# Optimization experiments

Measured on AMD Instinct MI355X. Metric: run time of the kernel, lower is better.

The kernel has to match this reference:

```python
import jax, jax.numpy as jnp
from jax import lax
import numpy as np

NEG = -1e30  # log-space -inf surrogate (avoids inf-inf NaNs)

def setup_inputs() -> dict:
    key = jax.random.key(0)
    k1, k2, k3, k4 = jax.random.split(key, 4)
    B, T, V, L = 32, 1024, 1024, 128
    logits = jax.random.normal(k1, (B, T, V), dtype=jnp.float32)
    targets = jax.random.randint(k2, (B, L), 1, V, dtype=jnp.int32)  # blank=0 excluded
    targets_lengths = jax.random.randint(k3, (B,), 64, L + 1, dtype=jnp.int32)
    logits_lengths = jax.random.randint(k4, (B,), 512, T + 1, dtype=jnp.int32)
    return {"logits": logits, "targets": targets,
            "logits_lengths": logits_lengths, "targets_lengths": targets_lengths}

def _ctc_neg_log_likelihood(logits, targets, logits_lengths, targets_lengths):
    # warp-ctc semantics: softmax applied internally, blank label = 0,
    # returns per-example negative log likelihood (reduce=False).
    B, T, V = logits.shape
    L = targets.shape[1]
    S = 2 * L + 1  # extended label seq: blank, l1, blank, l2, ..., blank
    logp = jax.nn.log_softmax(logits, axis=-1)            # [B,T,V]
    ext = jnp.zeros((B, S), jnp.int32).at[:, 1::2].set(targets)  # blanks at even s
    lp = jnp.take_along_axis(logp, ext[:, None, :], axis=2)      # [B,T,S]

    s_idx = jnp.arange(S)
    valid_s = s_idx[None, :] < (2 * targets_lengths[:, None] + 1)  # ragged label mask
    # skip transition s-2 -> s allowed only at non-blank s with ext[s] != ext[s-2]
    ext_m2 = jnp.pad(ext, ((0, 0), (2, 0)), constant_values=-1)[:, :S]
    can_skip = (s_idx[None, :] % 2 == 1) & (ext != ext_m2)

    alpha0 = jnp.full((B, S), NEG, logits.dtype)
    alpha0 = alpha0.at[:, 0].set(lp[:, 0, 0]).at[:, 1].set(lp[:, 0, 1])
    alpha0 = jnp.where(valid_s, alpha0, NEG)

    def step(alpha, inp):
        lp_t, t = inp  # lp_t: [B,S]
        a1 = alpha
        a2 = jnp.pad(alpha[:, :-1], ((0, 0), (1, 0)), constant_values=NEG)
        a3 = jnp.where(can_skip,
                       jnp.pad(alpha[:, :-2], ((0, 0), (2, 0)), constant_values=NEG),
                       NEG)
        m = jnp.maximum(jnp.maximum(a1, a2), a3)
        new = m + jnp.log(jnp.exp(a1 - m) + jnp.exp(a2 - m) + jnp.exp(a3 - m)) + lp_t
        new = jnp.where(valid_s, new, NEG)
        # freeze alpha past each example's logit length (ragged time)
        new = jnp.where((t < logits_lengths)[:, None], new, alpha)
        return new, None

    lp_time = jnp.swapaxes(lp, 0, 1)  # [T,B,S]
    alpha_T, _ = lax.scan(step, alpha0, (lp_time[1:], jnp.arange(1, T)))
    end_blank = jnp.take_along_axis(alpha_T, (2 * targets_lengths)[:, None], axis=1)[:, 0]
    end_label = jnp.take_along_axis(alpha_T, (2 * targets_lengths - 1)[:, None], axis=1)[:, 0]
    return -jnp.logaddexp(end_blank, end_label)  # [B]

def reference(logits, targets, logits_lengths, targets_lengths):
    return _ctc_neg_log_likelihood(logits, targets, logits_lengths, targets_lengths)
```

## Files before the change

kernel.cpp:

```cpp
#include <hip/hip_runtime.h>


#define LOG2E 1.4426950408889634f
#define LN2   0.6931471805599453f

constexpr int B = 32, T = 1024, V = 1024, L = 128;
constexpr int S = 2 * L + 1;
constexpr int TS = 64;

__device__ inline float fexp2(float x) { return __builtin_amdgcn_exp2f(x); }
__device__ inline float flog2(float x) { return __builtin_amdgcn_logf(x); }

template<int CTRL>
__device__ inline float dpp_mov(float old_, float x) {
    return __int_as_float(__builtin_amdgcn_update_dpp(
        __float_as_int(old_), __float_as_int(x), CTRL, 0xF, 0xF, false));
}

__global__ __launch_bounds__(256) void k_lse_gather(
    const float* __restrict__ logits, const int* __restrict__ targets,
    const int* __restrict__ tgtlen,
    float* __restrict__ pQ, float* __restrict__ pB)
{
    const int row = blockIdx.x;
    const int b   = row >> 10;
    const float* x = logits + (size_t)row * V;
    const int tid = threadIdx.x;

    float4 v = reinterpret_cast<const float4*>(x)[tid];
    float m = fmaxf(fmaxf(v.x, v.y), fmaxf(v.z, v.w));
    #pragma unroll
    for (int off = 32; off; off >>= 1) m = fmaxf(m, __shfl_xor(m, off));

    __shared__ float red[8];
    const int lane = tid & 63, wv = tid >> 6;
    if (lane == 0) red[wv] = m;
    __syncthreads();
    m = fmaxf(fmaxf(red[0], red[1]), fmaxf(red[2], red[3]));

    float s = fexp2((v.x - m) * LOG2E) + fexp2((v.y - m) * LOG2E)
            + fexp2((v.z - m) * LOG2E) + fexp2((v.w - m) * LOG2E);
    #pragma unroll
    for (int off = 32; off; off >>= 1) s += __shfl_xor(s, off);
    if (lane == 0) red[4 + wv] = s;
    __syncthreads();
    s = red[4] + red[5] + red[6] + red[7];

    const float lse2 = m * LOG2E + flog2(s);
    if (tid == 0) {
        pB[row] = fexp2(x[0] * LOG2E - lse2);
    } else if (tid <= L) {
        const int j  = tid - 1;
        const int tl = tgtlen[b];
        const int lab = targets[b * L + j];
        pQ[(size_t)row * 128 + j] =
            (j < tl) ? fexp2(x[lab] * LOG2E - lse2) : 0.0f;
    }
}

__global__ __launch_bounds__(64) void k_ctc_alpha(
    const float* __restrict__ pQ, const float* __restrict__ pB,
    const int* __restrict__ targets, const int* __restrict__ loglen,
    const int* __restrict__ tgtlen, float* __restrict__ out)
{
    const int b  = blockIdx.x;
    const int l  = threadIdx.x;
    const int len = loglen[b];
    const int tl  = tgtlen[b];

    const int* tg = targets + b * L;
    const int t2l   = tg[2 * l];
    const int t2lm1 = (l > 0) ? tg[2 * l - 1] : -3;
    const int t2lp1 = tg[2 * l + 1];
    const bool cs1 = (t2l != t2lm1);
    const bool cs3 = (t2lp1 != t2l);

    float A0 = (l == 0) ? pB[(size_t)b * T] : 0.0f;
    float A1 = (l == 0) ? pQ[(size_t)b * T * 128] : 0.0f;
    float A2 = 0.0f, A3 = 0.0f, A4 = 0.0f;
    float p3 = 0.0f;
    int Se = 0;

    __shared__ __align__(16) float sQ[2][TS][128];
    __shared__ __align__(16) float sB[2][TS];
    __shared__ float alpha[S];

    const float* gQ = pQ + (size_t)b * T * 128 + (l & 31) * 4;

    #define STAGE(buf, t0)                                                     \
    {                                                                          \
        _Pragma("unroll")                                                      \
        for (int c = 0; c < TS / 2; ++c) {                                     \
            const int r  = (t0) + 2 * c + (l >> 5);                            \
            const int rc = (r < T) ? r : (T - 1);                              \
            const float* gp = gQ + (size_t)rc * 128;                           \
            __builtin_amdgcn_global_load_lds(                                  \
                (const __attribute__((address_space(1))) void*)gp,             \
                (__attribute__((address_space(3))) void*)&sQ[buf][2 * c][0],   \
                16, 0, 0);                                                     \
        }                                                                      \
        {                                                                      \
            const int r  = (t0) + l;                                           \
            const int rc = (r < T) ? r : (T - 1);                              \
            const float* gp = pB + (size_t)b * T + rc;                         \
            __builtin_amdgcn_global_load_lds(                                  \
                (const __attribute__((address_space(1))) void*)gp,             \
                (__attribute__((address_space(3))) void*)&sB[buf][0],          \
                4, 0, 0);                                                      \
        }                                                                      \
    }

    float2 qa[8]; float ba[8];
    float2 qb[8]; float bbf[8];

    #define LOADG(QD, BD, cbuf, r0)                                            \
    {                                                                          \
        _Pragma("unroll")                                                      \
        for (int r = 0; r < 8; ++r) {                                          \
            QD[r] = *reinterpret_cast<const float2*>(&sQ[cbuf][(r0) + r][2*l]);\
            BD[r] = sB[cbuf][(r0) + r];                                        \
        }                                                                      \
    }

    #define STEP_ONE(pb, p1, pl3)                                              \
    {                                                                          \
        const float n0 = (A0 + p3) * (pb);                                     \
        const float n1 = (A1 + A0 + (cs1 ? p3 : 0.0f)) * (p1);                 \
        const float n2 = (A2 + A1) * (pb);                                     \
        const float n3 = (A3 + A2 + (cs3 ? A1 : 0.0f)) * (pl3);                \
        const float n4 = (A4 + A3) * (pb);                                     \
        A0 = n0; A1 = n1; A2 = n2; A3 = n3; A4 = n4;                           \
        p3 = dpp_mov<0x138>(0.0f, A3);             \
    }

    #define RESCALE()                                                          \
    {                                                                          \
        float m_ = fmaxf(fmaxf(A0, A1), fmaxf(A2, fmaxf(A3, A4)));             \
        m_ = fmaxf(m_, dpp_mov<0x111>(m_, m_));                \
        m_ = fmaxf(m_, dpp_mov<0x112>(m_, m_));                \
        m_ = fmaxf(m_, dpp_mov<0x114>(m_, m_));                \
        m_ = fmaxf(m_, dpp_mov<0x118>(m_, m_));                \
        m_ = fmaxf(m_, dpp_mov<0x142>(m_, m_));              \
        m_ = fmaxf(m_, dpp_mov<0x143>(m_, m_));              \
        const int e = (__builtin_amdgcn_readlane(__float_as_int(m_), 63)       \
                       >> 23) & 0xff;                                          \
        int kb = 374 - e;                       \
        if (kb > 254) kb = 254;                      \
        const float sc = __int_as_float(kb << 23);                             \
        A0 *= sc; A1 *= sc; A2 *= sc; A3 *= sc; A4 *= sc; p3 *= sc;            \
        Se -= (kb - 127);                                                      \
    }

    STAGE(0, 1);
    int cb = 0;

    int tb = 1;
    for (; tb + TS <= len; tb += TS) {
        asm volatile("s_waitcnt vmcnt(0)" ::: "memory");
        STAGE(cb ^ 1, tb + TS);
        LOADG(qa, ba, cb, 0);
        #pragma unroll
        for (int g = 0; g < 8; ++g) {
            if (g < 7) {
                if (g & 1) { LOADG(qa, ba, cb, (g + 1) * 8); }
                else       { LOADG(qb, bbf, cb, (g + 1) * 8); }
            }
            #pragma unroll
            for (int i = 0; i < 8; ++i) {
                if (g & 1) { STEP_ONE(bbf[i], qb[i].x, qb[i].y); }
                else       { STEP_ONE(ba[i],  qa[i].x, qa[i].y); }
            }
            RESCALE();
        }
        cb ^= 1;
    }
    if (tb < len) {
        asm volatile("s_waitcnt vmcnt(0)" ::: "memory");
        LOADG(qa, ba, cb, 0);
        #pragma unroll
        for (int g = 0; g < 8; ++g) {
            if (g < 7) {
                if (g & 1) { LOADG(qa, ba, cb, (g + 1) * 8); }
                else       { LOADG(qb, bbf, cb, (g + 1) * 8); }
            }
            #pragma unroll
            for (int i = 0; i < 8; ++i) {
                if (tb + g * 8 + i < len) {
                    if (g & 1) { STEP_ONE(bbf[i], qb[i].x, qb[i].y); }
                    else       { STEP_ONE(ba[i],  qa[i].x, qa[i].y); }
                }
            }
            if (tb + g * 8 + 7 < len) RESCALE();
        }
    }
    #undef STEP_ONE
    #undef RESCALE
    #undef LOADG
    #undef STAGE

    alpha[4 * l + 0] = A0;
    alpha[4 * l + 1] = A1;
    alpha[4 * l + 2] = A2;
    alpha[4 * l + 3] = A3;
    if (l == 63) alpha[256] = A4;
    __syncthreads();

    if (l == 0) {
        const float sum = alpha[2 * tl] + alpha[2 * tl - 1];
        out[b] = -LN2 * (flog2(sum) + (float)Se);
    }
}

extern "C" void kernel_launch(void* const* d_in, const int* in_sizes, int n_in,
                              void* d_out, int out_size, void* d_ws, size_t ws_size,
                              hipStream_t stream) {
    const float* logits  = (const float*)d_in[0];
    const int*   targets = (const int*)d_in[1];
    const int*   loglen  = (const int*)d_in[2];
    const int*   tgtlen  = (const int*)d_in[3];
    float* out = (float*)d_out;
    float* pQ = (float*)d_ws;
    float* pB = pQ + (size_t)B * T * 128;

    k_lse_gather<<<B * T, 256, 0, stream>>>(logits, targets, tgtlen, pQ, pB);
    k_ctc_alpha<<<B, 64, 0, stream>>>(pQ, pB, targets, loglen, tgtlen, out);
}
```

Before: 94.07 us.

## Pack eight batch recurrences per block and shrink the staging tile

```diff
diff --git a/kernel.cpp b/kernel.cpp
--- a/kernel.cpp
+++ b/kernel.cpp
@@ -6,7 +6,8 @@
 
 constexpr int B = 32, T = 1024, V = 1024, L = 128;
 constexpr int S = 2 * L + 1;
-constexpr int TS = 64;
+constexpr int TS = 16;
+constexpr int WPB = 8;
 
 __device__ inline float fexp2(float x) { return __builtin_amdgcn_exp2f(x); }
 __device__ inline float flog2(float x) { return __builtin_amdgcn_logf(x); }
@@ -58,13 +59,18 @@
     }
 }
 
-__global__ __launch_bounds__(64) void k_ctc_alpha(
+__global__ __launch_bounds__(512) void k_ctc_alpha(
     const float* __restrict__ pQ, const float* __restrict__ pB,
     const int* __restrict__ targets, const int* __restrict__ loglen,
     const int* __restrict__ tgtlen, float* __restrict__ out)
 {
-    const int b  = blockIdx.x;
-    const int l  = threadIdx.x;
+    __shared__ __align__(16) float sQ[WPB * 2 * TS * 128];
+    __shared__ __align__(16) float sB[WPB * 2 * 64];
+    __shared__ float al[WPB * (S + 3)];
+
+    const int l   = threadIdx.x & 63;
+    const int wid = __builtin_amdgcn_readfirstlane((int)(threadIdx.x >> 6));
+    const int b   = blockIdx.x * WPB + wid;
     const int len = loglen[b];
     const int tl  = tgtlen[b];
 
@@ -72,8 +78,8 @@
     const int t2l   = tg[2 * l];
     const int t2lm1 = (l > 0) ? tg[2 * l - 1] : -3;
     const int t2lp1 = tg[2 * l + 1];
-    const bool cs1 = (t2l != t2lm1);
-    const bool cs3 = (t2lp1 != t2l);
+    const float cs1f = (t2l != t2lm1) ? 1.0f : 0.0f;
+    const float cs3f = (t2lp1 != t2l) ? 1.0f : 0.0f;
 
     float A0 = (l == 0) ? pB[(size_t)b * T] : 0.0f;
     float A1 = (l == 0) ? pQ[(size_t)b * T * 128] : 0.0f;
@@ -81,11 +87,12 @@
     float p3 = 0.0f;
     int Se = 0;
 
-    __shared__ __align__(16) float sQ[2][TS][128];
-    __shared__ __align__(16) float sB[2][TS];
-    __shared__ float alpha[S];
+    float* sQw = sQ + wid * (2 * TS * 128);
+    float* sBw = sB + wid * (2 * 64);
+    float* alw = al + wid * (S + 3);
 
     const float* gQ = pQ + (size_t)b * T * 128 + (l & 31) * 4;
+    const float* gB = pB + (size_t)b * T;
 
     #define STAGE(buf, t0)                                                     \
     {                                                                          \
@@ -96,16 +103,18 @@
             const float* gp = gQ + (size_t)rc * 128;                           \
             __builtin_amdgcn_global_load_lds(                                  \
                 (const __attribute__((address_space(1))) void*)gp,             \
-                (__attribute__((address_space(3))) void*)&sQ[buf][2 * c][0],   \
+                (__attribute__((address_space(3))) void*)                      \
+                    (sQw + (buf) * (TS * 128) + 2 * c * 128),                  \
                 16, 0, 0);                                                     \
         }                                                                      \
         {                                                                      \
             const int r  = (t0) + l;                                           \
             const int rc = (r < T) ? r : (T - 1);                              \
-            const float* gp = pB + (size_t)b * T + rc;                         \
+            const float* gp = gB + rc;                                         \
             __builtin_amdgcn_global_load_lds(                                  \
                 (const __attribute__((address_space(1))) void*)gp,             \
-                (__attribute__((address_space(3))) void*)&sB[buf][0],          \
+                (__attribute__((address_space(3))) void*)                      \
+                    (sBw + (buf) * 64),                                        \
                 4, 0, 0);                                                      \
         }                                                                      \
     }
@@ -113,21 +122,22 @@
     float2 qa[8]; float ba[8];
     float2 qb[8]; float bbf[8];
 
-    #define LOADG(QD, BD, cbuf, r0)                                            \
+    #define LOADG(QD, BD, buf, r0)                                             \
     {                                                                          \
         _Pragma("unroll")                                                      \
         for (int r = 0; r < 8; ++r) {                                          \
-            QD[r] = *reinterpret_cast<const float2*>(&sQ[cbuf][(r0) + r][2*l]);\
-            BD[r] = sB[cbuf][(r0) + r];                                        \
+            QD[r] = *reinterpret_cast<const float2*>(                          \
+                sQw + (buf) * (TS * 128) + ((r0) + r) * 128 + 2 * l);          \
+            BD[r] = sBw[(buf) * 64 + (r0) + r];                                \
         }                                                                      \
     }
 
     #define STEP_ONE(pb, p1, pl3)                                              \
     {                                                                          \
         const float n0 = (A0 + p3) * (pb);                                     \
-        const float n1 = (A1 + A0 + (cs1 ? p3 : 0.0f)) * (p1);                 \
+        const float n1 = fmaf(cs1f, p3, A1 + A0) * (p1);                       \
         const float n2 = (A2 + A1) * (pb);                                     \
-        const float n3 = (A3 + A2 + (cs3 ? A1 : 0.0f)) * (pl3);                \
+        const float n3 = fmaf(cs3f, A1, A3 + A2) * (pl3);                      \
         const float n4 = (A4 + A3) * (pb);                                     \
         A0 = n0; A1 = n1; A2 = n2; A3 = n3; A4 = n4;                           \
         p3 = dpp_mov<0x138>(0.0f, A3);             \
@@ -159,38 +169,27 @@
         asm volatile("s_waitcnt vmcnt(0)" ::: "memory");
         STAGE(cb ^ 1, tb + TS);
         LOADG(qa, ba, cb, 0);
-        #pragma unroll
-        for (int g = 0; g < 8; ++g) {
-            if (g < 7) {
-                if (g & 1) { LOADG(qa, ba, cb, (g + 1) * 8); }
-                else       { LOADG(qb, bbf, cb, (g + 1) * 8); }
-            }
-            #pragma unroll
-            for (int i = 0; i < 8; ++i) {
-                if (g & 1) { STEP_ONE(bbf[i], qb[i].x, qb[i].y); }
-                else       { STEP_ONE(ba[i],  qa[i].x, qa[i].y); }
-            }
-            RESCALE();
-        }
+        LOADG(qb, bbf, cb, 8);
+        #pragma unroll
+        for (int i = 0; i < 8; ++i) { STEP_ONE(ba[i],  qa[i].x, qa[i].y); }
+        RESCALE();
+        #pragma unroll
+        for (int i = 0; i < 8; ++i) { STEP_ONE(bbf[i], qb[i].x, qb[i].y); }
+        RESCALE();
         cb ^= 1;
     }
     if (tb < len) {
         asm volatile("s_waitcnt vmcnt(0)" ::: "memory");
         LOADG(qa, ba, cb, 0);
-        #pragma unroll
-        for (int g = 0; g < 8; ++g) {
-            if (g < 7) {
-                if (g & 1) { LOADG(qa, ba, cb, (g + 1) * 8); }
-                else       { LOADG(qb, bbf, cb, (g + 1) * 8); }
-            }
-            #pragma unroll
-            for (int i = 0; i < 8; ++i) {
-                if (tb + g * 8 + i < len) {
-                    if (g & 1) { STEP_ONE(bbf[i], qb[i].x, qb[i].y); }
-                    else       { STEP_ONE(ba[i],  qa[i].x, qa[i].y); }
-                }
-            }
-            if (tb + g * 8 + 7 < len) RESCALE();
+        LOADG(qb, bbf, cb, 8);
+        #pragma unroll
+        for (int i = 0; i < 8; ++i) {
+            if (tb + i < len) { STEP_ONE(ba[i], qa[i].x, qa[i].y); }
+        }
+        if (tb + 7 < len) RESCALE();
+        #pragma unroll
+        for (int i = 0; i < 8; ++i) {
+            if (tb + 8 + i < len) { STEP_ONE(bbf[i], qb[i].x, qb[i].y); }
         }
     }
     #undef STEP_ONE
@@ -198,15 +197,15 @@
     #undef LOADG
     #undef STAGE
 
-    alpha[4 * l + 0] = A0;
-    alpha[4 * l + 1] = A1;
-    alpha[4 * l + 2] = A2;
-    alpha[4 * l + 3] = A3;
-    if (l == 63) alpha[256] = A4;
+    alw[4 * l + 0] = A0;
+    alw[4 * l + 1] = A1;
+    alw[4 * l + 2] = A2;
+    alw[4 * l + 3] = A3;
+    if (l == 63) alw[256] = A4;
     __syncthreads();
 
     if (l == 0) {
-        const float sum = alpha[2 * tl] + alpha[2 * tl - 1];
+        const float sum = alw[2 * tl] + alw[2 * tl - 1];
         out[b] = -LN2 * (flog2(sum) + (float)Se);
     }
 }
@@ -223,5 +222,6 @@
     float* pB = pQ + (size_t)B * T * 128;
 
     k_lse_gather<<<B * T, 256, 0, stream>>>(logits, targets, tgtlen, pQ, pB);
-    k_ctc_alpha<<<B, 64, 0, stream>>>(pQ, pB, targets, loglen, tgtlen, out);
-}
+    k_ctc_alpha<<<B / WPB, WPB * 64, 0, stream>>>(pQ, pB, targets, loglen,
+                                                  tgtlen, out);
+}
```

Measured after the change: 121.4 us. +29.1%, slower.

## Pair batch items by sorted logit length and interleave two CTC recurrences per wave

Applied to the files above, without the earlier changes.

```diff
diff --git a/kernel.cpp b/kernel.cpp
--- a/kernel.cpp
+++ b/kernel.cpp
@@ -6,7 +6,7 @@
 
 constexpr int B = 32, T = 1024, V = 1024, L = 128;
 constexpr int S = 2 * L + 1;
-constexpr int TS = 64;
+constexpr int TS = 16;
 
 __device__ inline float fexp2(float x) { return __builtin_amdgcn_exp2f(x); }
 __device__ inline float flog2(float x) { return __builtin_amdgcn_logf(x); }
@@ -58,84 +58,112 @@
     }
 }
 
-__global__ __launch_bounds__(64) void k_ctc_alpha(
+__global__ __launch_bounds__(64) void k_pair(const int* __restrict__ loglen,
+                                             int* __restrict__ perm)
+{
+    const int l = threadIdx.x;
+    int key = (l < B) ? (loglen[l] * 64 + l) : 0x7fffffff;
+    #pragma unroll
+    for (int k = 2; k <= 64; k <<= 1) {
+        #pragma unroll
+        for (int j = k >> 1; j >= 1; j >>= 1) {
+            const int other = __shfl_xor(key, j);
+            const bool dir = ((l & k) == 0);
+            const bool keepMin = (((l & j) == 0) == dir);
+            key = keepMin ? (other < key ? other : key)
+                          : (other > key ? other : key);
+        }
+    }
+    if (l < B) perm[l] = key & 63;
+}
+
+__global__ __launch_bounds__(64) void k_ctc_alpha2(
     const float* __restrict__ pQ, const float* __restrict__ pB,
     const int* __restrict__ targets, const int* __restrict__ loglen,
-    const int* __restrict__ tgtlen, float* __restrict__ out)
+    const int* __restrict__ tgtlen, const int* __restrict__ perm,
+    float* __restrict__ out)
 {
-    const int b  = blockIdx.x;
+    __shared__ __align__(16) float sQ[2 * 2 * TS * 128];
+    __shared__ __align__(16) float sB[2 * 2 * 64];
+    __shared__ float al[2][S + 3];
+
     const int l  = threadIdx.x;
-    const int len = loglen[b];
-    const int tl  = tgtlen[b];
-
-    const int* tg = targets + b * L;
-    const int t2l   = tg[2 * l];
-    const int t2lm1 = (l > 0) ? tg[2 * l - 1] : -3;
-    const int t2lp1 = tg[2 * l + 1];
-    const bool cs1 = (t2l != t2lm1);
-    const bool cs3 = (t2lp1 != t2l);
-
-    float A0 = (l == 0) ? pB[(size_t)b * T] : 0.0f;
-    float A1 = (l == 0) ? pQ[(size_t)b * T * 128] : 0.0f;
-    float A2 = 0.0f, A3 = 0.0f, A4 = 0.0f;
-    float p3 = 0.0f;
-    int Se = 0;
-
-    __shared__ __align__(16) float sQ[2][TS][128];
-    __shared__ __align__(16) float sB[2][TS];
-    __shared__ float alpha[S];
-
-    const float* gQ = pQ + (size_t)b * T * 128 + (l & 31) * 4;
-
-    #define STAGE(buf, t0)                                                     \
+    const int pA = __builtin_amdgcn_readfirstlane(perm[2 * blockIdx.x]);
+    const int pBt= __builtin_amdgcn_readfirstlane(perm[2 * blockIdx.x + 1]);
+
+    #define INIT(X, bval, slot)                                                \
+    const int b##X  = (bval);                                                  \
+    const int len##X = loglen[b##X];                                           \
+    const int tl##X  = tgtlen[b##X];                                           \
+    float cs1f##X, cs3f##X;                                                    \
+    { const int* tg = targets + b##X * L;                                      \
+      const int t2l   = tg[2 * l];                                             \
+      const int t2lm1 = (l > 0) ? tg[2 * l - 1] : -3;                          \
+      const int t2lp1 = tg[2 * l + 1];                                         \
+      cs1f##X = (t2l != t2lm1) ? 1.0f : 0.0f;                                  \
+      cs3f##X = (t2lp1 != t2l) ? 1.0f : 0.0f; }                                \
+    float A0##X = (l == 0) ? pB[(size_t)b##X * T] : 0.0f;                      \
+    float A1##X = (l == 0) ? pQ[(size_t)b##X * T * 128] : 0.0f;                \
+    float A2##X = 0.0f, A3##X = 0.0f, A4##X = 0.0f, p3##X = 0.0f;              \
+    int Se##X = 0;                                                             \
+    const float* gQ##X = pQ + (size_t)b##X * T * 128 + (l & 31) * 4;           \
+    const float* gB##X = pB + (size_t)b##X * T;                                \
+    float* sQw##X = sQ + (slot) * (2 * TS * 128);                              \
+    float* sBw##X = sB + (slot) * (2 * 64);                                    \
+    float2 q##X[8]; float bb##X[8];
+
+    INIT(A, pA, 0)
+    INIT(Z, pBt, 1)
+
+    #define STAGE(X, buf, t0)                                                  \
     {                                                                          \
         _Pragma("unroll")                                                      \
         for (int c = 0; c < TS / 2; ++c) {                                     \
             const int r  = (t0) + 2 * c + (l >> 5);                            \
             const int rc = (r < T) ? r : (T - 1);                              \
-            const float* gp = gQ + (size_t)rc * 128;                           \
+            const float* gp = gQ##X + (size_t)rc * 128;                        \
             __builtin_amdgcn_global_load_lds(                                  \
                 (const __attribute__((address_space(1))) void*)gp,             \
-                (__attribute__((address_space(3))) void*)&sQ[buf][2 * c][0],   \
-                16, 0, 0);                                                     \
+                (__attribute__((address_space(3))) void*)                      \
+                    (sQw##X + (buf) * (TS * 128) + 2 * c * 128), 16, 0, 0);    \
         }                                                                      \
-        {                                                                      \
-            const int r  = (t0) + l;                                           \
-            const int rc = (r < T) ? r : (T - 1);                              \
-            const float* gp = pB + (size_t)b * T + rc;                         \
-            __builtin_amdgcn_global_load_lds(                                  \
-                (const __attribute__((address_space(1))) void*)gp,             \
-                (__attribute__((address_space(3))) void*)&sB[buf][0],          \
-                4, 0, 0);                                                      \
-        }                                                                      \
-    }
-
-    float2 qa[8]; float ba[8];
-    float2 qb[8]; float bbf[8];
-
-    #define LOADG(QD, BD, cbuf, r0)                                            \
+        { const int r  = (t0) + (l & 15);                                      \
+          const int rc = (r < T) ? r : (T - 1);                                \
+          const float* gp = gB##X + rc;                                        \
+          __builtin_amdgcn_global_load_lds(                                    \
+              (const __attribute__((address_space(1))) void*)gp,               \
+              (__attribute__((address_space(3))) void*)(sBw##X + (buf) * 64),  \
+              4, 0, 0); }                                                      \
+    }
+
+    #define LOADG(X, buf, r0)                                                  \
     {                                                                          \
         _Pragma("unroll")                                                      \
         for (int r = 0; r < 8; ++r) {                                          \
-            QD[r] = *reinterpret_cast<const float2*>(&sQ[cbuf][(r0) + r][2*l]);\
-            BD[r] = sB[cbuf][(r0) + r];                                        \
+            q##X[r] = *reinterpret_cast<const float2*>(                        \
+                sQw##X + (buf) * (TS * 128) + ((r0) + r) * 128 + 2 * l);       \
+            bb##X[r] = sBw##X[(buf) * 64 + (r0) + r];                          \
         }                                                                      \
     }
 
-    #define STEP_ONE(pb, p1, pl3)                                              \
-    {                                                                          \
-        const float n0 = (A0 + p3) * (pb);                                     \
-        const float n1 = (A1 + A0 + (cs1 ? p3 : 0.0f)) * (p1);                 \
-        const float n2 = (A2 + A1) * (pb);                                     \
-        const float n3 = (A3 + A2 + (cs3 ? A1 : 0.0f)) * (pl3);                \
-        const float n4 = (A4 + A3) * (pb);                                     \
-        A0 = n0; A1 = n1; A2 = n2; A3 = n3; A4 = n4;                           \
-        p3 = dpp_mov<0x138>(0.0f, A3);             \
-    }
-
-    #define RESCALE()                                                          \
-    {                                                                          \
-        float m_ = fmaxf(fmaxf(A0, A1), fmaxf(A2, fmaxf(A3, A4)));             \
+    #define STEP(X, i)                                                         \
+    {                                                                          \
+        const float pbv = bb##X[i];                                            \
+        const float p1v = q##X[i].x;                                           \
+        const float p3v = q##X[i].y;                                           \
+        const float n0 = (A0##X + p3##X) * pbv;                                \
+        const float n1 = fmaf(cs1f##X, p3##X, A1##X + A0##X) * p1v;            \
+        const float n2 = (A2##X + A1##X) * pbv;                                \
+        const float n3 = fmaf(cs3f##X, A1##X, A3##X + A2##X) * p3v;            \
+        const float n4 = (A4##X + A3##X) * pbv;                                \
+        A0##X = n0; A1##X = n1; A2##X = n2; A3##X = n3; A4##X = n4;            \
+        p3##X = dpp_mov<0x138>(0.0f, A3##X);       \
+    }
+
+    #define RESCALE(X)                                                         \
+    {                                                                          \
+        float m_ = fmaxf(fmaxf(A0##X, A1##X),                                  \
+                         fmaxf(A2##X, fmaxf(A3##X, A4##X)));                   \
         m_ = fmaxf(m_, dpp_mov<0x111>(m_, m_));                \
         m_ = fmaxf(m_, dpp_mov<0x112>(m_, m_));                \
         m_ = fmaxf(m_, dpp_mov<0x114>(m_, m_));                \
@@ -147,67 +175,77 @@
         int kb = 374 - e;                       \
         if (kb > 254) kb = 254;                      \
         const float sc = __int_as_float(kb << 23);                             \
-        A0 *= sc; A1 *= sc; A2 *= sc; A3 *= sc; A4 *= sc; p3 *= sc;            \
-        Se -= (kb - 127);                                                      \
-    }
-
-    STAGE(0, 1);
+        A0##X *= sc; A1##X *= sc; A2##X *= sc; A3##X *= sc; A4##X *= sc;       \
+        p3##X *= sc;                                                           \
+        Se##X -= (kb - 127);                                                   \
+    }
+
+    STAGE(A, 0, 1); STAGE(Z, 0, 1);
     int cb = 0;
-
     int tb = 1;
-    for (; tb + TS <= len; tb += TS) {
+
+    for (; tb + TS <= lenA; tb += TS) {
         asm volatile("s_waitcnt vmcnt(0)" ::: "memory");
-        STAGE(cb ^ 1, tb + TS);
-        LOADG(qa, ba, cb, 0);
-        #pragma unroll
-        for (int g = 0; g < 8; ++g) {
-            if (g < 7) {
-                if (g & 1) { LOADG(qa, ba, cb, (g + 1) * 8); }
-                else       { LOADG(qb, bbf, cb, (g + 1) * 8); }
-            }
-            #pragma unroll
-            for (int i = 0; i < 8; ++i) {
-                if (g & 1) { STEP_ONE(bbf[i], qb[i].x, qb[i].y); }
-                else       { STEP_ONE(ba[i],  qa[i].x, qa[i].y); }
-            }
-            RESCALE();
-        }
+        STAGE(A, cb ^ 1, tb + TS); STAGE(Z, cb ^ 1, tb + TS);
+        LOADG(A, cb, 0); LOADG(Z, cb, 0);
+        #pragma unroll
+        for (int i = 0; i < 8; ++i) { STEP(A, i); STEP(Z, i); }
+        RESCALE(A); RESCALE(Z);
+        LOADG(A, cb, 8); LOADG(Z, cb, 8);
+        #pragma unroll
+        for (int i = 0; i < 8; ++i) { STEP(A, i); STEP(Z, i); }
+        RESCALE(A); RESCALE(Z);
         cb ^= 1;
     }
-    if (tb < len) {
+
+    int cbA = cb;
+    for (int t2 = tb; t2 < lenA; t2 += TS) {
         asm volatile("s_waitcnt vmcnt(0)" ::: "memory");
-        LOADG(qa, ba, cb, 0);
-        #pragma unroll
-        for (int g = 0; g < 8; ++g) {
-            if (g < 7) {
-                if (g & 1) { LOADG(qa, ba, cb, (g + 1) * 8); }
-                else       { LOADG(qb, bbf, cb, (g + 1) * 8); }
-            }
-            #pragma unroll
-            for (int i = 0; i < 8; ++i) {
-                if (tb + g * 8 + i < len) {
-                    if (g & 1) { STEP_ONE(bbf[i], qb[i].x, qb[i].y); }
-                    else       { STEP_ONE(ba[i],  qa[i].x, qa[i].y); }
-                }
-            }
-            if (tb + g * 8 + 7 < len) RESCALE();
-        }
-    }
-    #undef STEP_ONE
+        STAGE(A, cbA ^ 1, t2 + TS);
+        LOADG(A, cbA, 0);
+        #pragma unroll
+        for (int i = 0; i < 8; ++i) { if (t2 + i < lenA) STEP(A, i); }
+        if (t2 + 7 < lenA) RESCALE(A);
+        LOADG(A, cbA, 8);
+        #pragma unroll
+        for (int i = 0; i < 8; ++i) { if (t2 + 8 + i < lenA) STEP(A, i); }
+        if (t2 + 15 < lenA) RESCALE(A);
+        cbA ^= 1;
+    }
+
+    int cbZ = cb;
+    for (int t2 = tb; t2 < lenZ; t2 += TS) {
+        asm volatile("s_waitcnt vmcnt(0)" ::: "memory");
+        STAGE(Z, cbZ ^ 1, t2 + TS);
+        LOADG(Z, cbZ, 0);
+        #pragma unroll
+        for (int i = 0; i < 8; ++i) { if (t2 + i < lenZ) STEP(Z, i); }
+        if (t2 + 7 < lenZ) RESCALE(Z);
+        LOADG(Z, cbZ, 8);
+        #pragma unroll
+        for (int i = 0; i < 8; ++i) { if (t2 + 8 + i < lenZ) STEP(Z, i); }
+        if (t2 + 15 < lenZ) RESCALE(Z);
+        cbZ ^= 1;
+    }
+
+    #undef STEP
     #undef RESCALE
     #undef LOADG
     #undef STAGE
-
-    alpha[4 * l + 0] = A0;
-    alpha[4 * l + 1] = A1;
-    alpha[4 * l + 2] = A2;
-    alpha[4 * l + 3] = A3;
-    if (l == 63) alpha[256] = A4;
+    #undef INIT
+
+    al[0][4 * l + 0] = A0A; al[0][4 * l + 1] = A1A;
+    al[0][4 * l + 2] = A2A; al[0][4 * l + 3] = A3A;
+    al[1][4 * l + 0] = A0Z; al[1][4 * l + 1] = A1Z;
+    al[1][4 * l + 2] = A2Z; al[1][4 * l + 3] = A3Z;
+    if (l == 63) { al[0][256] = A4A; al[1][256] = A4Z; }
     __syncthreads();
 
     if (l == 0) {
-        const float sum = alpha[2 * tl] + alpha[2 * tl - 1];
-        out[b] = -LN2 * (flog2(sum) + (float)Se);
+        float sum = al[0][2 * tlA] + al[0][2 * tlA - 1];
+        out[bA] = -LN2 * (flog2(sum) + (float)SeA);
+        sum = al[1][2 * tlZ] + al[1][2 * tlZ - 1];
+        out[bZ] = -LN2 * (flog2(sum) + (float)SeZ);
     }
 }
 
@@ -221,7 +259,10 @@
     float* out = (float*)d_out;
     float* pQ = (float*)d_ws;
     float* pB = pQ + (size_t)B * T * 128;
+    int*   perm = (int*)(pB + (size_t)B * T);
 
     k_lse_gather<<<B * T, 256, 0, stream>>>(logits, targets, tgtlen, pQ, pB);
-    k_ctc_alpha<<<B, 64, 0, stream>>>(pQ, pB, targets, loglen, tgtlen, out);
-}
+    k_pair<<<1, 64, 0, stream>>>(loglen, perm);
+    k_ctc_alpha2<<<B / 2, 64, 0, stream>>>(pQ, pB, targets, loglen, tgtlen,
+                                           perm, out);
+}
```

New measurement: 147.9 us. 57.2% more time.
